# Optimization experiments

Measured on AMD Instinct MI355X. Metric: run time of the kernel, lower is better.

## Reference

```python
import jax, jax.numpy as jnp
import numpy as np
import math

D, H, S, B, E, FF = 768, 12, 1024, 2, 32768, 4 * 768
HD = D // H


def layer_norm(x, g, b, eps=1e-5):
    m = jnp.mean(x, axis=-1, keepdims=True)
    v = jnp.mean((x - m) ** 2, axis=-1, keepdims=True)
    return (x - m) / jnp.sqrt(v + eps) * g + b


def setup_inputs() -> dict:
    key = jax.random.key(0)
    ks = jax.random.split(key, 24)
    w = lambda k, shape: jax.random.normal(k, shape, dtype=jnp.float32) * 0.02
    inp = {
        "x": jax.random.normal(ks[0], (B, S, D), dtype=jnp.float32),
        "adj_mask": jax.random.randint(ks[1], (B, S, S), 0, 2).astype(bool),
        "edge_attr": jax.random.normal(ks[2], (E,), dtype=jnp.float32),
        "edge_index": jax.random.randint(ks[3], (2, E), 0, S),
        "norm1_g": jnp.ones((D,), jnp.float32),
        "norm1_b": jnp.zeros((D,), jnp.float32),
        "Wq": w(ks[4], (D, D)), "bq": jnp.zeros((D,), jnp.float32),
        "Wk": w(ks[5], (D, D)), "bk": jnp.zeros((D,), jnp.float32),
        "Wv": w(ks[6], (D, D)), "bv": jnp.zeros((D,), jnp.float32),
        "Wo": w(ks[7], (D, D)), "bo": jnp.zeros((D,), jnp.float32),
        "norm2_g": jnp.ones((D,), jnp.float32),
        "norm2_b": jnp.zeros((D,), jnp.float32),
        "mlp_W1": w(ks[8], (D, FF)), "mlp_b1": jnp.zeros((FF,), jnp.float32),
        "mlp_W2": w(ks[9], (FF, D)), "mlp_b2": jnp.zeros((D,), jnp.float32),
        # per-head edge-attr MLP: Linear(1,16) -> GELU -> Linear(16,1), stacked over H heads
        "ep_W1": w(ks[10], (H, 16)), "ep_b1": jnp.zeros((H, 16), jnp.float32),
        "ep_W2": w(ks[11], (H, 16)), "ep_b2": jnp.zeros((H,), jnp.float32),
    }
    return inp


def reference(x, adj_mask, edge_attr, edge_index,
              norm1_g, norm1_b, Wq, bq, Wk, bk, Wv, bv, Wo, bo,
              norm2_g, norm2_b, mlp_W1, mlp_b1, mlp_W2, mlp_b2,
              ep_W1, ep_b1, ep_W2, ep_b2):
    Bb, Ss, Dd = x.shape
    Hh = ep_W1.shape[0]
    hd = Dd // Hh
    residual = x
    nx = layer_norm(x, norm1_g, norm1_b)
    q = (nx @ Wq + bq).reshape(Bb, Ss, Hh, hd).transpose(0, 2, 1, 3)  # [B,H,S,hd]
    k = (nx @ Wk + bk).reshape(Bb, Ss, Hh, hd).transpose(0, 2, 1, 3)
    v = (nx @ Wv + bv).reshape(Bb, Ss, Hh, hd).transpose(0, 2, 1, 3)
    scores = jnp.einsum('bhqd,bhkd->bhqk', q, k) / math.sqrt(hd)
    mask = adj_mask.astype(bool)[:, None]  # [B,1,S,S]
    scores = jnp.where(mask, scores, jnp.float32(-1e9))
    # per-edge per-head bias (computed under no_grad in the original -> stop_gradient)
    h1 = jax.nn.gelu(edge_attr[:, None, None] * ep_W1[None] + ep_b1[None], approximate=False)  # [E,H,16]
    proj = jnp.einsum('ehk,hk->eh', h1, ep_W2) + ep_b2  # [E,H]
    proj = jax.lax.stop_gradient(proj)
    src, dst = edge_index[0], edge_index[1]
    bias = jnp.zeros((Hh, Ss, Ss), x.dtype).at[:, src, dst].set(proj.T)  # [H,S,S]
    scores = scores + jnp.where(mask, bias[None], jnp.float32(0.0))
    attn = jax.nn.softmax(scores, axis=-1)
    out = jnp.einsum('bhqk,bhkd->bhqd', attn, v)
    out = out.transpose(0, 2, 1, 3).reshape(Bb, Ss, Dd)
    x = residual + (out @ Wo + bo)
    y = layer_norm(x, norm2_g, norm2_b)
    y = jax.nn.gelu(y @ mlp_W1 + mlp_b1, approximate=False) @ mlp_W2 + mlp_b2
    return x + y
```

## Files before the change

### kernel.cpp

```cpp
#include <hip/hip_runtime.h>
#include <hip/hip_bf16.h>

#define B_ 2
#define S_ 1024
#define D_ 768
#define H_ 12
#define HD_ 64
#define FF_ 3072
#define E_ 32768
#define QS_ 2304
#define NSPLIT 4
#define NSPLIT_W2 4
#define BHS (B_ * H_ * S_)

typedef short bf16x8 __attribute__((ext_vector_type(8)));
typedef float f32x4 __attribute__((ext_vector_type(4)));

#define SW(row, seg) ((((seg) ^ ((row) & 7)) * 8))

__device__ __forceinline__ unsigned short f2bf(float f) {
    __hip_bfloat16 h = __float2bfloat16(f);
    return __builtin_bit_cast(unsigned short, h);
}
__device__ __forceinline__ float bf2f(unsigned short u) {
    unsigned int v = ((unsigned int)u) << 16;
    return __builtin_bit_cast(float, v);
}
__device__ __forceinline__ float gelu_exact(float x) {
    return 0.5f * x * (1.0f + erff(x * 0.70710678118654752f));
}
__device__ __forceinline__ void gload_lds16(const unsigned short* g, unsigned short* l) {
    __builtin_amdgcn_global_load_lds((const __attribute__((address_space(1))) void*)g,
                                     (__attribute__((address_space(3))) void*)l, 16, 0, 0);
}

__global__ __launch_bounds__(256) void prep_kernel(
    const void* __restrict__ adj, unsigned int* __restrict__ mp, int* __restrict__ winner,
    const float* __restrict__ Wq, const float* __restrict__ Wk, const float* __restrict__ Wv,
    const float* __restrict__ Wo, const float* __restrict__ W1, const float* __restrict__ W2,
    unsigned short* __restrict__ wqkvt, unsigned short* __restrict__ wot,
    unsigned short* __restrict__ w1t, unsigned short* __restrict__ w2t,
    const float* __restrict__ bq, const float* __restrict__ bk, const float* __restrict__ bv,
    float* __restrict__ bqkv,
    const float* __restrict__ x, const float* __restrict__ g1, const float* __restrict__ bn1,
    unsigned short* __restrict__ nxb)
{
    __shared__ float tile[32][33];
    __shared__ unsigned int words[32];
    __shared__ int u8f;
    __shared__ float red[8];
    const int blk = blockIdx.x;
    const int t = threadIdx.x;

    if (blk < 2048) {
        const int b = blk >> 10, q = blk & 1023;
        if (b == 0) {
            int4 v; v.x = -1; v.y = -1; v.z = -1; v.w = -1;
            reinterpret_cast<int4*>(winner)[q * 256 + t] = v;
        }
        if (t < 32) words[t] = 0;
        if (t == 0) u8f = 0;
        __syncthreads();
        const unsigned int* row8 = (const unsigned int*)((const unsigned char*)adj + ((size_t)b * S_ + q) * S_);
        const unsigned int* row32 = (const unsigned int*)((const int*)adj + ((size_t)b * S_ + q) * S_);
        const unsigned int v = row8[t];
        if (v & 0xFF00FF00u) atomicOr(&u8f, 1);
        __syncthreads();
        if (u8f) {
            unsigned int nib = 0;
            if (v & 0x000000FFu) nib |= 1u;
            if (v & 0x0000FF00u) nib |= 2u;
            if (v & 0x00FF0000u) nib |= 4u;
            if (v & 0xFF000000u) nib |= 8u;
            if (nib) atomicOr(&words[t >> 3], nib << ((t & 7) * 4));
        } else {
            for (int i = 0; i < 4; i++) {
                const int k = i * 256 + t;
                if (row32[k]) atomicOr(&words[k >> 5], 1u << (k & 31));
            }
        }
        __syncthreads();
        if (t < 32) mp[((size_t)b * S_ + q) * 32 + t] = words[t];
    } else if (blk < 8960) {
        const int w = blk - 2048;
        const float* src; unsigned short* dst; int K, N, nb, kb;
        if (w < 2304) {
            const int z = w / 576, r = w - z * 576;
            K = 768; N = 768; kb = (r / 24) * 32; nb = (r % 24) * 32;
            src = (z == 0) ? Wq : (z == 1) ? Wk : (z == 2) ? Wv : Wo;
            dst = (z == 3) ? wot : wqkvt + (size_t)z * 768 * 768;
        } else if (w < 4608) {
            const int r = w - 2304;
            K = 768; N = 3072; nb = (r % 96) * 32; kb = (r / 96) * 32;
            src = W1; dst = w1t;
        } else {
            const int r = w - 4608;
            K = 3072; N = 768; kb = (r % 96) * 32; nb = (r / 96) * 32;
            src = W2; dst = w2t;
        }
        const int tx = t & 31, ty = t >> 5;
        for (int r = 0; r < 32; r += 8)
            tile[ty + r][tx] = src[(size_t)(kb + ty + r) * N + nb + tx];
        __syncthreads();
        for (int r = 0; r < 32; r += 8)
            dst[(size_t)(nb + ty + r) * K + kb + tx] = f2bf(tile[tx][ty + r]);
        if (w == 0) {
            for (int i = t; i < QS_; i += 256)
                bqkv[i] = (i < 768) ? bq[i] : (i < 1536) ? bk[i - 768] : bv[i - 1536];
        }
    } else {
        const int row = blk - 8960;
        const float* xr = x + (size_t)row * D_;
        float v0 = xr[t], v1 = xr[t + 256], v2 = xr[t + 512];
        float s = v0 + v1 + v2, s2 = v0 * v0 + v1 * v1 + v2 * v2;
        for (int m = 32; m; m >>= 1) { s += __shfl_xor(s, m); s2 += __shfl_xor(s2, m); }
        const int w = t >> 6;
        if ((t & 63) == 0) { red[w] = s; red[4 + w] = s2; }
        __syncthreads();
        s = red[0] + red[1] + red[2] + red[3];
        s2 = red[4] + red[5] + red[6] + red[7];
        const float mean = s * (1.f / D_);
        const float var = s2 * (1.f / D_) - mean * mean;
        const float rstd = rsqrtf(var + 1e-5f);
        unsigned short* orow = nxb + (size_t)row * D_;
        orow[t]       = f2bf((v0 - mean) * rstd * g1[t]       + bn1[t]);
        orow[t + 256] = f2bf((v1 - mean) * rstd * g1[t + 256] + bn1[t + 256]);
        orow[t + 512] = f2bf((v2 - mean) * rstd * g1[t + 512] + bn1[t + 512]);
    }
}

__global__ __launch_bounds__(256) void ln_kernel(
    const float* __restrict__ x, const float* __restrict__ g,
    const float* __restrict__ b, unsigned short* __restrict__ out)
{
    const int row = blockIdx.x;
    const int t = threadIdx.x;
    const float* xr = x + (size_t)row * D_;
    float v0 = xr[t], v1 = xr[t + 256], v2 = xr[t + 512];
    float s = v0 + v1 + v2, s2 = v0 * v0 + v1 * v1 + v2 * v2;
    for (int m = 32; m; m >>= 1) { s += __shfl_xor(s, m); s2 += __shfl_xor(s2, m); }
    __shared__ float red[8];
    const int w = t >> 6;
    if ((t & 63) == 0) { red[w] = s; red[4 + w] = s2; }
    __syncthreads();
    s = red[0] + red[1] + red[2] + red[3];
    s2 = red[4] + red[5] + red[6] + red[7];
    const float mean = s * (1.f / D_);
    const float var = s2 * (1.f / D_) - mean * mean;
    const float rstd = rsqrtf(var + 1e-5f);
    unsigned short* orow = out + (size_t)row * D_;
    orow[t]       = f2bf((v0 - mean) * rstd * g[t]       + b[t]);
    orow[t + 256] = f2bf((v1 - mean) * rstd * g[t + 256] + b[t + 256]);
    orow[t + 512] = f2bf((v2 - mean) * rstd * g[t + 512] + b[t + 512]);
}

__global__ __launch_bounds__(256) void edge_proj_scatter_kernel(
    const float* __restrict__ ea, const float* __restrict__ W1, const float* __restrict__ b1,
    const float* __restrict__ W2, const float* __restrict__ b2,
    const int* __restrict__ ei, float* __restrict__ proj, int* __restrict__ winner)
{
    const int tid = blockIdx.x * 256 + threadIdx.x;
    const int e = tid / H_, h = tid - e * H_;
    const float a = ea[e];
    float s = 0.f;
    for (int j = 0; j < 16; j++) {
        const float tv = a * W1[h * 16 + j] + b1[h * 16 + j];
        s += gelu_exact(tv) * W2[h * 16 + j];
    }
    proj[tid] = s + b2[h];
    if (h == 0) {
        const int sn = ei[e], dn = ei[E_ + e];
        atomicMax(&winner[sn * S_ + dn], e);
    }
}

__global__ __launch_bounds__(256) void qkv_kernel(
    const unsigned short* __restrict__ A, const unsigned short* __restrict__ Bt,
    const float* __restrict__ bias, unsigned short* __restrict__ qkv,
    unsigned short* __restrict__ vt,
    const int* __restrict__ winner, const float* __restrict__ proj,
    unsigned short* __restrict__ ebias)
{
    const int blk = blockIdx.x;
    const int t = threadIdx.x;
    if (blk >= 288) {
        const int q = blk - 288;
        const int k4 = t * 4;
        const int4 wv = *reinterpret_cast<const int4*>(&winner[q * S_ + k4]);
        for (int h = 0; h < H_; h++) {
            unsigned int lo = 0, hi = 0;
            if (wv.x >= 0) lo |= (unsigned int)f2bf(proj[(size_t)wv.x * H_ + h]);
            if (wv.y >= 0) lo |= ((unsigned int)f2bf(proj[(size_t)wv.y * H_ + h])) << 16;
            if (wv.z >= 0) hi |= (unsigned int)f2bf(proj[(size_t)wv.z * H_ + h]);
            if (wv.w >= 0) hi |= ((unsigned int)f2bf(proj[(size_t)wv.w * H_ + h])) << 16;
            uint2 val; val.x = lo; val.y = hi;
            *reinterpret_cast<uint2*>(&ebias[((size_t)h * S_ + q) * S_ + k4]) = val;
        }
        return;
    }
    __shared__ unsigned short As[128][64];
    __shared__ unsigned short Bs[128][64];
    const int bx = blk % 18, by = blk / 18;
    const int m0 = by * 128, n0 = bx * 128;
    const int w = t >> 6, l = t & 63;
    const int wm = w >> 1, wn = w & 1;
    const int lr = l & 15, g = l >> 4;
    const int lrow8 = l >> 3;
    const int lseg = (l & 7) ^ lrow8;
    f32x4 acc[4][4] = {};
    for (int k0 = 0; k0 < D_; k0 += 64) {
        __syncthreads();
        for (int j = 0; j < 4; j++) {
            const int q = w * 4 + j;
            const int row = q * 8 + lrow8;
            gload_lds16(A  + (size_t)(m0 + row) * D_ + k0 + lseg * 8, &As[q * 8][0]);
            gload_lds16(Bt + (size_t)(n0 + row) * D_ + k0 + lseg * 8, &Bs[q * 8][0]);
        }
        __syncthreads();
        for (int kk = 0; kk < 2; kk++) {
            bf16x8 af[4], bfr[4];
            for (int m = 0; m < 4; m++) {
                const int r = wm * 64 + m * 16 + lr;
                af[m] = *reinterpret_cast<const bf16x8*>(&As[r][SW(r, kk * 4 + g)]);
            }
            for (int n = 0; n < 4; n++) {
                const int r = wn * 64 + n * 16 + lr;
                bfr[n] = *reinterpret_cast<const bf16x8*>(&Bs[r][SW(r, kk * 4 + g)]);
            }
            for (int m = 0; m < 4; m++)
                for (int n = 0; n < 4; n++)
                    acc[m][n] = __builtin_amdgcn_mfma_f32_16x16x32_bf16(af[m], bfr[n], acc[m][n], 0, 0, 0);
        }
    }
    if (n0 >= 1536) {
        for (int m = 0; m < 4; m++)
            for (int n = 0; n < 4; n++) {
                const int col = n0 + wn * 64 + n * 16 + lr;
                const int vcol = col - 1536;
                const int hh = vcol >> 6, d = vcol & 63;
                const float bvv = bias[col];
                const int grow = m0 + wm * 64 + m * 16 + g * 4;
                const int bb = grow >> 10, s = grow & 1023;
                ushort4 o;
                o.x = f2bf(acc[m][n][0] + bvv);
                o.y = f2bf(acc[m][n][1] + bvv);
                o.z = f2bf(acc[m][n][2] + bvv);
                o.w = f2bf(acc[m][n][3] + bvv);
                *reinterpret_cast<ushort4*>(&vt[(((size_t)(bb * H_ + hh) * HD_) + d) * S_ + s]) = o;
            }
    } else {
        for (int m = 0; m < 4; m++)
            for (int n = 0; n < 4; n++) {
                const int col = n0 + wn * 64 + n * 16 + lr;
                const float scl = (col < 768) ? 0.125f : 1.0f;
                const float bvv = bias[col];
                for (int j = 0; j < 4; j++) {
                    const int row = m0 + wm * 64 + m * 16 + g * 4 + j;
                    qkv[(size_t)row * QS_ + col] = f2bf((acc[m][n][j] + bvv) * scl);
                }
            }
    }
}

template<bool RES, bool OUTBF>
__global__ __launch_bounds__(256) void gemm_kernel(
    const unsigned short* __restrict__ A, const unsigned short* __restrict__ Bt,
    const float* __restrict__ bias, const float* __restrict__ res,
    void* __restrict__ outp, int M, int N, int K)
{
    __shared__ unsigned short As[64][40];
    __shared__ unsigned short Bs[64][40];
    const int m0 = blockIdx.y * 64, n0 = blockIdx.x * 64;
    const int t = threadIdx.x;
    const int w = t >> 6, l = t & 63;
    const int wm = w >> 1, wn = w & 1;
    const int r = l & 15, g = l >> 4;
    const int srow = t >> 2, sseg = t & 3;
    f32x4 acc[2][2] = {};
    for (int k0 = 0; k0 < K; k0 += 32) {
        __syncthreads();
        const uint4 av = *reinterpret_cast<const uint4*>(A + (size_t)(m0 + srow) * K + k0 + sseg * 8);
        *reinterpret_cast<uint4*>(&As[srow][sseg * 8]) = av;
        const uint4 bv = *reinterpret_cast<const uint4*>(Bt + (size_t)(n0 + srow) * K + k0 + sseg * 8);
        *reinterpret_cast<uint4*>(&Bs[srow][sseg * 8]) = bv;
        __syncthreads();
        bf16x8 af[2], bfr[2];
        af[0]  = *reinterpret_cast<const bf16x8*>(&As[wm * 32 + r][g * 8]);
        af[1]  = *reinterpret_cast<const bf16x8*>(&As[wm * 32 + 16 + r][g * 8]);
        bfr[0] = *reinterpret_cast<const bf16x8*>(&Bs[wn * 32 + r][g * 8]);
        bfr[1] = *reinterpret_cast<const bf16x8*>(&Bs[wn * 32 + 16 + r][g * 8]);
        for (int m = 0; m < 2; m++)
            for (int n = 0; n < 2; n++)
                acc[m][n] = __builtin_amdgcn_mfma_f32_16x16x32_bf16(af[m], bfr[n], acc[m][n], 0, 0, 0);
    }
    for (int m = 0; m < 2; m++)
        for (int n = 0; n < 2; n++) {
            const int col = n0 + wn * 32 + n * 16 + r;
            const float bvv = bias[col];
            for (int j = 0; j < 4; j++) {
                const int row = m0 + wm * 32 + m * 16 + g * 4 + j;
                float v = acc[m][n][j] + bvv;
                if (RES) v += res[(size_t)row * N + col];
                if (OUTBF) ((unsigned short*)outp)[(size_t)row * N + col] = f2bf(v);
                else       ((float*)outp)[(size_t)row * N + col] = v;
            }
        }
}

template<bool GELU, bool OUTBF, bool SPLITK>
__global__ __launch_bounds__(256) void gemm128_kernel(
    const unsigned short* __restrict__ A, const unsigned short* __restrict__ Bt,
    const float* __restrict__ bias, void* __restrict__ outp,
    int M, int N, int K, int klen, int scale_below)
{
    __shared__ unsigned short As[128][64];
    __shared__ unsigned short Bs[128][64];
    const int m0 = blockIdx.y * 128, n0 = blockIdx.x * 128;
    const int t = threadIdx.x;
    const int w = t >> 6, l = t & 63;
    const int wm = w >> 1, wn = w & 1;
    const int lr = l & 15, g = l >> 4;
    const int lrow8 = l >> 3;
    const int lseg = (l & 7) ^ lrow8;
    const int kbeg = SPLITK ? blockIdx.z * klen : 0;
    const int kend = SPLITK ? kbeg + klen : K;
    f32x4 acc[4][4] = {};
    for (int k0 = kbeg; k0 < kend; k0 += 64) {
        __syncthreads();
        for (int j = 0; j < 4; j++) {
            const int q = w * 4 + j;
            const int row = q * 8 + lrow8;
            gload_lds16(A  + (size_t)(m0 + row) * K + k0 + lseg * 8, &As[q * 8][0]);
            gload_lds16(Bt + (size_t)(n0 + row) * K + k0 + lseg * 8, &Bs[q * 8][0]);
        }
        __syncthreads();
        for (int kk = 0; kk < 2; kk++) {
            bf16x8 af[4], bfr[4];
            for (int m = 0; m < 4; m++) {
                const int r = wm * 64 + m * 16 + lr;
                af[m] = *reinterpret_cast<const bf16x8*>(&As[r][SW(r, kk * 4 + g)]);
            }
            for (int n = 0; n < 4; n++) {
                const int r = wn * 64 + n * 16 + lr;
                bfr[n] = *reinterpret_cast<const bf16x8*>(&Bs[r][SW(r, kk * 4 + g)]);
            }
            for (int m = 0; m < 4; m++)
                for (int n = 0; n < 4; n++)
                    acc[m][n] = __builtin_amdgcn_mfma_f32_16x16x32_bf16(af[m], bfr[n], acc[m][n], 0, 0, 0);
        }
    }
    if (SPLITK) {
        for (int m = 0; m < 4; m++)
            for (int n = 0; n < 4; n++) {
                const int col = n0 + wn * 64 + n * 16 + lr;
                for (int j = 0; j < 4; j++) {
                    const int row = m0 + wm * 64 + m * 16 + g * 4 + j;
                    if (OUTBF) ((unsigned short*)outp)[((size_t)blockIdx.z * M + row) * N + col] = f2bf(acc[m][n][j]);
                    else       ((float*)outp)[((size_t)blockIdx.z * M + row) * N + col] = acc[m][n][j];
                }
            }
    } else {
        for (int m = 0; m < 4; m++)
            for (int n = 0; n < 4; n++) {
                const int col = n0 + wn * 64 + n * 16 + lr;
                const float scl = (col < scale_below) ? 0.125f : 1.0f;
                const float bvv = bias[col];
                for (int j = 0; j < 4; j++) {
                    const int row = m0 + wm * 64 + m * 16 + g * 4 + j;
                    float v = (acc[m][n][j] + bvv) * scl;
                    if (GELU) v = gelu_exact(v);
                    if (OUTBF) ((unsigned short*)outp)[(size_t)row * N + col] = f2bf(v);
                    else       ((float*)outp)[(size_t)row * N + col] = v;
                }
            }
    }
}

__global__ __launch_bounds__(256) void w2_reduce_kernel(
    const unsigned short* __restrict__ part, const float* __restrict__ x2,
    const float* __restrict__ b2, float* __restrict__ out)
{
    const int idx = (blockIdx.x * 256 + threadIdx.x) * 4;
    const int col = idx % D_;
    const float4 xr = *reinterpret_cast<const float4*>(&x2[idx]);
    const float4 bb = *reinterpret_cast<const float4*>(&b2[col]);
    float4 o;
    o.x = xr.x + bb.x; o.y = xr.y + bb.y; o.z = xr.z + bb.z; o.w = xr.w + bb.w;
    for (int s = 0; s < NSPLIT_W2; s++) {
        const uint2 p = *reinterpret_cast<const uint2*>(&part[(size_t)s * B_ * S_ * D_ + idx]);
        o.x += bf2f((unsigned short)(p.x & 0xFFFF));
        o.y += bf2f((unsigned short)(p.x >> 16));
        o.z += bf2f((unsigned short)(p.y & 0xFFFF));
        o.w += bf2f((unsigned short)(p.y >> 16));
    }
    *reinterpret_cast<float4*>(&out[idx]) = o;
}

__global__ __launch_bounds__(256) void attn_mfma_kernel(
    const unsigned short* __restrict__ qkv,
    const unsigned short* __restrict__ vt,
    const unsigned short* __restrict__ ebias,
    const unsigned int* __restrict__ mp,
    unsigned short* __restrict__ pacc,
    float2* __restrict__ pml)
{
    __shared__ unsigned short Ks[64][64];
    __shared__ unsigned short Vs[64][64];
    __shared__ unsigned short Eb[64][72];
    __shared__ unsigned int   Mw[64][2];
    __shared__ unsigned short Ps[4][16][64];
    const int t = threadIdx.x;
    const int w = t >> 6, l = t & 63;
    const int lr = l & 15, g = l >> 4;
    const int qt = blockIdx.x & 15, sp = blockIdx.x >> 4;
    const int q0 = qt * 64;
    const int h = blockIdx.y, b = blockIdx.z;
    const int bh = b * H_ + h;
    const size_t qbase = (size_t)b * S_ * QS_ + h * HD_;
    const size_t kbase = qbase + 768;
    const size_t vtbase = (size_t)bh * HD_ * S_;

    const int qrow = q0 + w * 16 + lr;
    const bf16x8 af0 = *reinterpret_cast<const bf16x8*>(qkv + qbase + (size_t)qrow * QS_ + g * 8);
    const bf16x8 af1 = *reinterpret_cast<const bf16x8*>(qkv + qbase + (size_t)qrow * QS_ + 32 + g * 8);

    float m_run[4], l_run[4];
    f32x4 acc[4] = {};
    for (int j = 0; j < 4; j++) { m_run[j] = -3.0e38f; l_run[j] = 0.f; }

    const int srow = t >> 2, sseg = t & 3;
    const int kt_beg = sp * (S_ / NSPLIT), kt_end = kt_beg + S_ / NSPLIT;
    for (int kt = kt_beg; kt < kt_end; kt += 64) {
        __syncthreads();
        {
            const unsigned short* ksrc = qkv + kbase + (size_t)(kt + srow) * QS_ + sseg * 16;
            *reinterpret_cast<uint4*>(&Ks[srow][SW(srow, sseg * 2)])     = *reinterpret_cast<const uint4*>(ksrc);
            *reinterpret_cast<uint4*>(&Ks[srow][SW(srow, sseg * 2 + 1)]) = *reinterpret_cast<const uint4*>(ksrc + 8);
            const unsigned short* vsrc = vt + vtbase + (size_t)srow * S_ + kt + sseg * 16;
            *reinterpret_cast<uint4*>(&Vs[srow][SW(srow, sseg * 2)])     = *reinterpret_cast<const uint4*>(vsrc);
            *reinterpret_cast<uint4*>(&Vs[srow][SW(srow, sseg * 2 + 1)]) = *reinterpret_cast<const uint4*>(vsrc + 8);
            const unsigned short* esrc = ebias + ((size_t)h * S_ + q0 + srow) * S_ + kt + sseg * 16;
            *reinterpret_cast<uint4*>(&Eb[srow][sseg * 16])     = *reinterpret_cast<const uint4*>(esrc);
            *reinterpret_cast<uint4*>(&Eb[srow][sseg * 16 + 8]) = *reinterpret_cast<const uint4*>(esrc + 8);
            if (t < 128) Mw[t >> 1][t & 1] = mp[((size_t)b * S_ + q0 + (t >> 1)) * 32 + (kt >> 5) + (t & 1)];
        }
        __syncthreads();
        f32x4 sc[4];
        for (int n = 0; n < 4; n++) {
            const int r = n * 16 + lr;
            const bf16x8 b0 = *reinterpret_cast<const bf16x8*>(&Ks[r][SW(r, g)]);
            const bf16x8 b1 = *reinterpret_cast<const bf16x8*>(&Ks[r][SW(r, 4 + g)]);
            f32x4 z = {};
            z = __builtin_amdgcn_mfma_f32_16x16x32_bf16(af0, b0, z, 0, 0, 0);
            z = __builtin_amdgcn_mfma_f32_16x16x32_bf16(af1, b1, z, 0, 0, 0);
            sc[n] = z;
        }
        float tmax[4] = {-3.0e38f, -3.0e38f, -3.0e38f, -3.0e38f};
        for (int n = 0; n < 4; n++) {
            for (int j = 0; j < 4; j++) {
                const int rq = w * 16 + g * 4 + j;
                const unsigned int word = Mw[rq][n >> 1];
                const bool msk = (word >> ((n & 1) * 16 + lr)) & 1;
                float sval;
                if (msk) sval = sc[n][j] + bf2f(Eb[rq][n * 16 + lr]);
                else sval = -1e9f;
                sc[n][j] = sval;
                tmax[j] = fmaxf(tmax[j], sval);
            }
        }
        float pscale[4];
        for (int j = 0; j < 4; j++) {
            float tm = tmax[j];
            tm = fmaxf(tm, __shfl_xor(tm, 1));
            tm = fmaxf(tm, __shfl_xor(tm, 2));
            tm = fmaxf(tm, __shfl_xor(tm, 4));
            tm = fmaxf(tm, __shfl_xor(tm, 8));
            const float mnew = fmaxf(m_run[j], tm);
            pscale[j] = __expf(m_run[j] - mnew);
            m_run[j] = mnew;
            l_run[j] *= pscale[j];
        }
        float psum[4] = {0.f, 0.f, 0.f, 0.f};
        for (int n = 0; n < 4; n++) {
            for (int j = 0; j < 4; j++) {
                const float p = __expf(sc[n][j] - m_run[j]);
                psum[j] += p;
                const int row = g * 4 + j;
                Ps[w][row][SW(row, n * 2 + (lr >> 3)) + (lr & 7)] = f2bf(p);
            }
        }
        for (int j = 0; j < 4; j++) {
            float s = psum[j];
            s += __shfl_xor(s, 1); s += __shfl_xor(s, 2);
            s += __shfl_xor(s, 4); s += __shfl_xor(s, 8);
            l_run[j] += s;
            for (int n2 = 0; n2 < 4; n2++) acc[n2][j] *= pscale[j];
        }
        const bf16x8 pa0 = *reinterpret_cast<const bf16x8*>(&Ps[w][lr][SW(lr, g)]);
        const bf16x8 pa1 = *reinterpret_cast<const bf16x8*>(&Ps[w][lr][SW(lr, 4 + g)]);
        for (int n2 = 0; n2 < 4; n2++) {
            const int r = n2 * 16 + lr;
            const bf16x8 vb0 = *reinterpret_cast<const bf16x8*>(&Vs[r][SW(r, g)]);
            const bf16x8 vb1 = *reinterpret_cast<const bf16x8*>(&Vs[r][SW(r, 4 + g)]);
            acc[n2] = __builtin_amdgcn_mfma_f32_16x16x32_bf16(pa0, vb0, acc[n2], 0, 0, 0);
            acc[n2] = __builtin_amdgcn_mfma_f32_16x16x32_bf16(pa1, vb1, acc[n2], 0, 0, 0);
        }
    }
    const size_t prow = (size_t)sp * BHS + (size_t)bh * S_;
    for (int j = 0; j < 4; j++) {
        const int qg = q0 + w * 16 + g * 4 + j;
        for (int n2 = 0; n2 < 4; n2++)
            pacc[(prow + qg) * 64 + n2 * 16 + lr] = f2bf(acc[n2][j]);
        if (lr == 0) { float2 v; v.x = m_run[j]; v.y = l_run[j]; pml[prow + qg] = v; }
    }
}

__global__ __launch_bounds__(256) void attn_combine_kernel(
    const unsigned short* __restrict__ pacc, const float2* __restrict__ pml,
    unsigned short* __restrict__ attnb)
{
    const int idx = (blockIdx.x * 256 + threadIdx.x) * 4;
    const int r = idx >> 6, d = idx & 63;
    float2 ml[NSPLIT];
    float mx = -3.0e38f;
    for (int s = 0; s < NSPLIT; s++) {
        ml[s] = pml[(size_t)s * BHS + r];
        mx = fmaxf(mx, ml[s].x);
    }
    float wgt[NSPLIT], L = 0.f;
    for (int s = 0; s < NSPLIT; s++) {
        wgt[s] = __expf(ml[s].x - mx);
        L += ml[s].y * wgt[s];
    }
    const float inv = (L > 0.f) ? 1.f / L : 0.f;
    float4 o = {0.f, 0.f, 0.f, 0.f};
    for (int s = 0; s < NSPLIT; s++) {
        const uint2 p = *reinterpret_cast<const uint2*>(&pacc[((size_t)s * BHS + r) * 64 + d]);
        o.x += bf2f((unsigned short)(p.x & 0xFFFF)) * wgt[s];
        o.y += bf2f((unsigned short)(p.x >> 16)) * wgt[s];
        o.z += bf2f((unsigned short)(p.y & 0xFFFF)) * wgt[s];
        o.w += bf2f((unsigned short)(p.y >> 16)) * wgt[s];
    }
    const int bh = r >> 10, q = r & 1023;
    const int b = bh / H_, h = bh - b * H_;
    ushort4 ov;
    ov.x = f2bf(o.x * inv); ov.y = f2bf(o.y * inv);
    ov.z = f2bf(o.z * inv); ov.w = f2bf(o.w * inv);
    *reinterpret_cast<ushort4*>(&attnb[((size_t)(b * S_ + q)) * D_ + h * HD_ + d]) = ov;
}

extern "C" void kernel_launch(void* const* d_in, const int* in_sizes, int n_in,
                              void* d_out, int out_size, void* d_ws, size_t ws_size,
                              hipStream_t stream)
{
    const float* x    = (const float*)d_in[0];
    const void*  adj  = d_in[1];
    const float* ea   = (const float*)d_in[2];
    const int*   ei   = (const int*)d_in[3];
    const float* g1   = (const float*)d_in[4];
    const float* bn1  = (const float*)d_in[5];
    const float* Wq   = (const float*)d_in[6];
    const float* bq   = (const float*)d_in[7];
    const float* Wk   = (const float*)d_in[8];
    const float* bk   = (const float*)d_in[9];
    const float* Wv   = (const float*)d_in[10];
    const float* bv   = (const float*)d_in[11];
    const float* Wo   = (const float*)d_in[12];
    const float* bo   = (const float*)d_in[13];
    const float* g2   = (const float*)d_in[14];
    const float* bn2  = (const float*)d_in[15];
    const float* W1   = (const float*)d_in[16];
    const float* mb1  = (const float*)d_in[17];
    const float* W2   = (const float*)d_in[18];
    const float* mb2  = (const float*)d_in[19];
    const float* epW1 = (const float*)d_in[20];
    const float* epb1 = (const float*)d_in[21];
    const float* epW2 = (const float*)d_in[22];
    const float* epb2 = (const float*)d_in[23];

    char* ws = (char*)d_ws;
    size_t off = 0;
    auto carve = [&](size_t bytes) -> void* {
        void* p = ws + off;
        off += (bytes + 255) & ~(size_t)255;
        return p;
    };
    unsigned short* wqkvt = (unsigned short*)carve((size_t)QS_ * D_ * 2);
    unsigned short* wot   = (unsigned short*)carve((size_t)D_ * D_ * 2);
    unsigned short* w1t   = (unsigned short*)carve((size_t)FF_ * D_ * 2);
    unsigned short* w2t   = (unsigned short*)carve((size_t)D_ * FF_ * 2);
    float*          bqkv  = (float*)carve((size_t)QS_ * 4);
    float*          proj  = (float*)carve((size_t)E_ * H_ * 4);
    int*            winner= (int*)carve((size_t)S_ * S_ * 4);
    unsigned short* ebias = (unsigned short*)carve((size_t)H_ * S_ * S_ * 2);
    unsigned int*   mpk   = (unsigned int*)carve((size_t)B_ * S_ * 32 * 4);
    unsigned short* nxb   = (unsigned short*)carve((size_t)B_ * S_ * D_ * 2);
    unsigned short* attnb = (unsigned short*)carve((size_t)B_ * S_ * D_ * 2);
    unsigned short* qkv   = (unsigned short*)carve((size_t)B_ * S_ * QS_ * 2);
    unsigned short* vtb   = (unsigned short*)carve((size_t)B_ * S_ * D_ * 2);
    float*          x2f   = (float*)carve((size_t)B_ * S_ * D_ * 4);
    unsigned short* pacc  = (unsigned short*)carve((size_t)NSPLIT * BHS * 64 * 2);
    float2*         pml   = (float2*)carve((size_t)NSPLIT * BHS * 8);
    unsigned short* ln2b = nxb;
    unsigned short* hb   = qkv;
    unsigned short* pw2  = (unsigned short*)ebias;

    const int M = B_ * S_;

    prep_kernel<<<11008, 256, 0, stream>>>(
        adj, mpk, winner,
        Wq, Wk, Wv, Wo, W1, W2, wqkvt, wot, w1t, w2t, bq, bk, bv, bqkv,
        x, g1, bn1, nxb);

    edge_proj_scatter_kernel<<<(E_ * H_) / 256, 256, 0, stream>>>(
        ea, epW1, epb1, epW2, epb2, ei, proj, winner);

    qkv_kernel<<<288 + S_, 256, 0, stream>>>(
        nxb, wqkvt, bqkv, qkv, vtb, winner, proj, ebias);

    attn_mfma_kernel<<<dim3(16 * NSPLIT, H_, B_), 256, 0, stream>>>(
        qkv, vtb, ebias, mpk, pacc, pml);
    attn_combine_kernel<<<(BHS * 64) / 1024, 256, 0, stream>>>(pacc, pml, attnb);

    gemm_kernel<true, false><<<dim3(D_ / 64, M / 64), 256, 0, stream>>>(
        attnb, wot, bo, x, x2f, M, D_, D_);

    ln_kernel<<<M, 256, 0, stream>>>(x2f, g2, bn2, ln2b);

    gemm128_kernel<true, true, false><<<dim3(FF_ / 128, M / 128), 256, 0, stream>>>(
        ln2b, w1t, mb1, hb, M, FF_, D_, D_, 0);
    gemm128_kernel<false, true, true><<<dim3(D_ / 128, M / 128, NSPLIT_W2), 256, 0, stream>>>(
        hb, w2t, mb2, pw2, M, D_, FF_, FF_ / NSPLIT_W2, 0);
    w2_reduce_kernel<<<(M * D_) / 1024, 256, 0, stream>>>(pw2, x2f, mb2, (float*)d_out);
}
```

Measured before the change: 183.6 us.

## Fuse W2 split-K reduction via atomics and prefetch attention tiles into registers

The W2 split-K GEMM now atomically adds fp32 partials straight into the output. The output is pre-initialised with residual plus bias inside the second layernorm kernel, which removes the separate reduce kernel and the bf16 partial buffer. Separately, the attention kernel loads the next K/V/bias/mask tile into registers while the current tile is being computed, a software-pipelined prefetch. Atomics add contention and make the summation order nondeterministic, and the prefetch raises register pressure.

Result: slower. 194.3 us (+5.9%).

```diff
diff --git a/kernel.cpp b/kernel.cpp
--- a/kernel.cpp
+++ b/kernel.cpp
@@ -129,9 +129,10 @@
     }
 }
 
-__global__ __launch_bounds__(256) void ln_kernel(
+__global__ __launch_bounds__(256) void ln2_kernel(
     const float* __restrict__ x, const float* __restrict__ g,
-    const float* __restrict__ b, unsigned short* __restrict__ out)
+    const float* __restrict__ b, unsigned short* __restrict__ out,
+    const float* __restrict__ b2, float* __restrict__ dinit)
 {
     const int row = blockIdx.x;
     const int t = threadIdx.x;
@@ -152,6 +153,10 @@
     orow[t]       = f2bf((v0 - mean) * rstd * g[t]       + b[t]);
     orow[t + 256] = f2bf((v1 - mean) * rstd * g[t + 256] + b[t + 256]);
     orow[t + 512] = f2bf((v2 - mean) * rstd * g[t + 512] + b[t + 512]);
+    float* drow = dinit + (size_t)row * D_;
+    drow[t]       = v0 + b2[t];
+    drow[t + 256] = v1 + b2[t + 256];
+    drow[t + 512] = v2 + b2[t + 512];
 }
 
 __global__ __launch_bounds__(256) void edge_proj_scatter_kernel(
@@ -307,7 +312,7 @@
         }
 }
 
-template<bool GELU, bool OUTBF, bool SPLITK>
+template<bool GELU, bool OUTBF, bool SPLITK, bool ATOMIC>
 __global__ __launch_bounds__(256) void gemm128_kernel(
     const unsigned short* __restrict__ A, const unsigned short* __restrict__ Bt,
     const float* __restrict__ bias, void* __restrict__ outp,
@@ -355,8 +360,13 @@
                 const int col = n0 + wn * 64 + n * 16 + lr;
                 for (int j = 0; j < 4; j++) {
                     const int row = m0 + wm * 64 + m * 16 + g * 4 + j;
-                    if (OUTBF) ((unsigned short*)outp)[((size_t)blockIdx.z * M + row) * N + col] = f2bf(acc[m][n][j]);
-                    else       ((float*)outp)[((size_t)blockIdx.z * M + row) * N + col] = acc[m][n][j];
+                    if (ATOMIC) {
+                        atomicAdd((float*)outp + (size_t)row * N + col, acc[m][n][j]);
+                    } else if (OUTBF) {
+                        ((unsigned short*)outp)[((size_t)blockIdx.z * M + row) * N + col] = f2bf(acc[m][n][j]);
+                    } else {
+                        ((float*)outp)[((size_t)blockIdx.z * M + row) * N + col] = acc[m][n][j];
+                    }
                 }
             }
     } else {
@@ -374,26 +384,6 @@
                 }
             }
     }
-}
-
-__global__ __launch_bounds__(256) void w2_reduce_kernel(
-    const unsigned short* __restrict__ part, const float* __restrict__ x2,
-    const float* __restrict__ b2, float* __restrict__ out)
-{
-    const int idx = (blockIdx.x * 256 + threadIdx.x) * 4;
-    const int col = idx % D_;
-    const float4 xr = *reinterpret_cast<const float4*>(&x2[idx]);
-    const float4 bb = *reinterpret_cast<const float4*>(&b2[col]);
-    float4 o;
-    o.x = xr.x + bb.x; o.y = xr.y + bb.y; o.z = xr.z + bb.z; o.w = xr.w + bb.w;
-    for (int s = 0; s < NSPLIT_W2; s++) {
-        const uint2 p = *reinterpret_cast<const uint2*>(&part[(size_t)s * B_ * S_ * D_ + idx]);
-        o.x += bf2f((unsigned short)(p.x & 0xFFFF));
-        o.y += bf2f((unsigned short)(p.x >> 16));
-        o.z += bf2f((unsigned short)(p.y & 0xFFFF));
-        o.w += bf2f((unsigned short)(p.y >> 16));
-    }
-    *reinterpret_cast<float4*>(&out[idx]) = o;
 }
 
 __global__ __launch_bounds__(256) void attn_mfma_kernel(
@@ -430,21 +420,36 @@
 
     const int srow = t >> 2, sseg = t & 3;
     const int kt_beg = sp * (S_ / NSPLIT), kt_end = kt_beg + S_ / NSPLIT;
+
+    uint4 kr0, kr1, vr0, vr1, er0, er1;
+    unsigned int mr = 0;
+    auto load_tile = [&](int kt) {
+        const unsigned short* ksrc = qkv + kbase + (size_t)(kt + srow) * QS_ + sseg * 16;
+        kr0 = *reinterpret_cast<const uint4*>(ksrc);
+        kr1 = *reinterpret_cast<const uint4*>(ksrc + 8);
+        const unsigned short* vsrc = vt + vtbase + (size_t)srow * S_ + kt + sseg * 16;
+        vr0 = *reinterpret_cast<const uint4*>(vsrc);
+        vr1 = *reinterpret_cast<const uint4*>(vsrc + 8);
+        const unsigned short* esrc = ebias + ((size_t)h * S_ + q0 + srow) * S_ + kt + sseg * 16;
+        er0 = *reinterpret_cast<const uint4*>(esrc);
+        er1 = *reinterpret_cast<const uint4*>(esrc + 8);
+        if (t < 128) mr = mp[((size_t)b * S_ + q0 + (t >> 1)) * 32 + (kt >> 5) + (t & 1)];
+    };
+    load_tile(kt_beg);
+
     for (int kt = kt_beg; kt < kt_end; kt += 64) {
         __syncthreads();
         {
-            const unsigned short* ksrc = qkv + kbase + (size_t)(kt + srow) * QS_ + sseg * 16;
-            *reinterpret_cast<uint4*>(&Ks[srow][SW(srow, sseg * 2)])     = *reinterpret_cast<const uint4*>(ksrc);
-            *reinterpret_cast<uint4*>(&Ks[srow][SW(srow, sseg * 2 + 1)]) = *reinterpret_cast<const uint4*>(ksrc + 8);
-            const unsigned short* vsrc = vt + vtbase + (size_t)srow * S_ + kt + sseg * 16;
-            *reinterpret_cast<uint4*>(&Vs[srow][SW(srow, sseg * 2)])     = *reinterpret_cast<const uint4*>(vsrc);
-            *reinterpret_cast<uint4*>(&Vs[srow][SW(srow, sseg * 2 + 1)]) = *reinterpret_cast<const uint4*>(vsrc + 8);
-            const unsigned short* esrc = ebias + ((size_t)h * S_ + q0 + srow) * S_ + kt + sseg * 16;
-            *reinterpret_cast<uint4*>(&Eb[srow][sseg * 16])     = *reinterpret_cast<const uint4*>(esrc);
-            *reinterpret_cast<uint4*>(&Eb[srow][sseg * 16 + 8]) = *reinterpret_cast<const uint4*>(esrc + 8);
-            if (t < 128) Mw[t >> 1][t & 1] = mp[((size_t)b * S_ + q0 + (t >> 1)) * 32 + (kt >> 5) + (t & 1)];
-        }
-        __syncthreads();
+            *reinterpret_cast<uint4*>(&Ks[srow][SW(srow, sseg * 2)])     = kr0;
+            *reinterpret_cast<uint4*>(&Ks[srow][SW(srow, sseg * 2 + 1)]) = kr1;
+            *reinterpret_cast<uint4*>(&Vs[srow][SW(srow, sseg * 2)])     = vr0;
+            *reinterpret_cast<uint4*>(&Vs[srow][SW(srow, sseg * 2 + 1)]) = vr1;
+            *reinterpret_cast<uint4*>(&Eb[srow][sseg * 16])     = er0;
+            *reinterpret_cast<uint4*>(&Eb[srow][sseg * 16 + 8]) = er1;
+            if (t < 128) Mw[t >> 1][t & 1] = mr;
+        }
+        __syncthreads();
+        if (kt + 64 < kt_end) load_tile(kt + 64);
         f32x4 sc[4];
         for (int n = 0; n < 4; n++) {
             const int r = n * 16 + lr;
@@ -603,7 +608,6 @@
     float2*         pml   = (float2*)carve((size_t)NSPLIT * BHS * 8);
     unsigned short* ln2b = nxb;
     unsigned short* hb   = qkv;
-    unsigned short* pw2  = (unsigned short*)ebias;
 
     const int M = B_ * S_;
 
@@ -625,11 +629,10 @@
     gemm_kernel<true, false><<<dim3(D_ / 64, M / 64), 256, 0, stream>>>(
         attnb, wot, bo, x, x2f, M, D_, D_);
 
-    ln_kernel<<<M, 256, 0, stream>>>(x2f, g2, bn2, ln2b);
-
-    gemm128_kernel<true, true, false><<<dim3(FF_ / 128, M / 128), 256, 0, stream>>>(
+    ln2_kernel<<<M, 256, 0, stream>>>(x2f, g2, bn2, ln2b, mb2, (float*)d_out);
+
+    gemm128_kernel<true, true, false, false><<<dim3(FF_ / 128, M / 128), 256, 0, stream>>>(
         ln2b, w1t, mb1, hb, M, FF_, D_, D_, 0);
-    gemm128_kernel<false, true, true><<<dim3(D_ / 128, M / 128, NSPLIT_W2), 256, 0, stream>>>(
-        hb, w2t, mb2, pw2, M, D_, FF_, FF_ / NSPLIT_W2, 0);
-    w2_reduce_kernel<<<(M * D_) / 1024, 256, 0, stream>>>(pw2, x2f, mb2, (float*)d_out);
-}
+    gemm128_kernel<false, false, true, true><<<dim3(D_ / 128, M / 128, NSPLIT_W2), 256, 0, stream>>>(
+        hb, w2t, mb2, (float*)d_out, M, D_, FF_, FF_ / NSPLIT_W2, 0);
+}
```
